# Kernel optimization log

Hardware: AMD Instinct MI355X
Metric: run time of the kernel (lower is better)

Reference implementation:

```python
import jax, jax.numpy as jnp
import numpy as np

N, F, H, F_ = 8192, 256, 2, 64
NEG_MASK = -1e10
LEAKY_SLOPE = 0.2


def setup_inputs() -> dict:
    key = jax.random.key(0)
    k0, k1, k2, k3 = jax.random.split(key, 4)
    X = jax.random.normal(k0, (N, F), jnp.float32)
    A = (jax.random.uniform(k1, (N, N)) < 0.01).astype(jnp.float32)
    A = jnp.maximum(A, jnp.eye(N, dtype=jnp.float32))
    W = jax.random.normal(k2, (H, F, F_), jnp.float32) * (1.0 / np.sqrt(F))
    b = jnp.zeros((H, F_), jnp.float32)
    a = jax.random.normal(k3, (H, F_), jnp.float32) * 0.1
    return {"X": X, "A": A, "W": W, "b": b, "a": a}


def reference(X, A, W, b, a):
    # per-head projected features: [H, N, F_]
    feats = jnp.einsum('nf,hfo->hno', X, W)
    # score[h,i,j] = sum_o feats[h,i,o] * feats[h,j,o] * a[h,o]
    # (identical math to Dot(axes=-1)([X_0*X_1, a^T]) without the [N,N,F_] tensor)
    scores = jnp.einsum('hno,hmo->hnm', feats * a[:, None, :], feats)
    scores = jax.nn.leaky_relu(scores, negative_slope=LEAKY_SLOPE)
    scores = scores + NEG_MASK * (1.0 - A)  # adjacency mask (broadcast over heads)
    attn = jax.nn.softmax(scores, axis=-1)  # [H, N, N]
    # dropout_rate=0 -> identity at inference
    out = jnp.einsum('hnm,hmo->hno', attn, feats) + b[:, None, :]  # [H, N, F_]
    out = jnp.transpose(out, (1, 0, 2)).reshape(X.shape[0], H * F_)  # concat heads
    return jax.nn.relu(out)
```

## Files before the change

kernel.cpp:

```cpp
#include <hip/hip_runtime.h>

#define NN 8192
#define FIN 256
#define FO 64
#define CAP 192

typedef float nf4 __attribute__((ext_vector_type(4)));

__global__ __launch_bounds__(256) void feats_kernel(
    const float* __restrict__ X,
    const float* __restrict__ W,
    float* __restrict__ feats)
{
    __shared__ float Ws[128*FO];
    __shared__ float Xs[32*132];
    const int h = blockIdx.y;
    const int row0 = blockIdx.x * 32;
    const int t = threadIdx.x;
    const int rg = t >> 4;
    const int c0 = (t & 15) << 2;
    float acc0[4] = {0.f,0.f,0.f,0.f};
    float acc1[4] = {0.f,0.f,0.f,0.f};

    for (int kp = 0; kp < 2; ++kp){
        const int kb = kp * 128;
        const float* Wh = W + h*FIN*FO + kb*FO;
        #pragma unroll
        for (int it=0; it<8; ++it){
            int flat = (it*256 + t)*4;
            *(float4*)&Ws[flat] = *(const float4*)&Wh[flat];
        }
        #pragma unroll
        for (int it=0; it<4; ++it){
            int flat = (it*256 + t)*4;
            int r = flat >> 7, f0 = flat & 127;
            *(float4*)&Xs[r*132 + f0] = *(const float4*)&X[(size_t)(row0+r)*FIN + kb + f0];
        }
        __syncthreads();
        const float* xp0 = &Xs[(rg*2+0)*132];
        const float* xp1 = &Xs[(rg*2+1)*132];
        #pragma unroll 4
        for (int k=0; k<128; ++k){
            float x0 = xp0[k], x1 = xp1[k];
            float4 w4 = *(const float4*)&Ws[k*FO + c0];
            acc0[0]=fmaf(x0,w4.x,acc0[0]); acc0[1]=fmaf(x0,w4.y,acc0[1]);
            acc0[2]=fmaf(x0,w4.z,acc0[2]); acc0[3]=fmaf(x0,w4.w,acc0[3]);
            acc1[0]=fmaf(x1,w4.x,acc1[0]); acc1[1]=fmaf(x1,w4.y,acc1[1]);
            acc1[2]=fmaf(x1,w4.z,acc1[2]); acc1[3]=fmaf(x1,w4.w,acc1[3]);
        }
        __syncthreads();
    }
    float* o0 = feats + ((size_t)(row0 + rg*2 + 0)*2 + h)*FO + c0;
    float* o1 = feats + ((size_t)(row0 + rg*2 + 1)*2 + h)*FO + c0;
    *(float4*)o0 = make_float4(acc0[0],acc0[1],acc0[2],acc0[3]);
    *(float4*)o1 = make_float4(acc1[0],acc1[1],acc1[2],acc1[3]);
}

__global__ __launch_bounds__(512) void gat_kernel(
    const float* __restrict__ A,
    const float* __restrict__ feats,
    const float* __restrict__ av,
    const float* __restrict__ bv,
    float* __restrict__ out)
{
    __shared__ int   nsh[CAP];
    __shared__ float s0[CAP], s1[CAP];
    __shared__ float part[8*128];
    __shared__ float red[2];
    __shared__ int   s_c;

    const int i = blockIdx.x, t = threadIdx.x;
    const int l  = t & 63;
    const int wv = t >> 6;
    const int gi = t >> 5, l32 = t & 31;

    float4 qa = *(const float4*)&av[l32*4];
    float4 qf = *(const float4*)&feats[(size_t)i*128 + l32*4];
    const float4 q4 = make_float4(qf.x*qa.x, qf.y*qa.y, qf.z*qa.z, qf.w*qa.w);

    if (t == 0) s_c = 0;
    __syncthreads();

    const nf4* Arow4 = (const nf4*)(A + (size_t)i*NN);
    nf4 v[4];
    #pragma unroll
    for (int r=0; r<4; ++r) v[r] = __builtin_nontemporal_load(&Arow4[r*512 + t]);

    const unsigned long long ltmask = (1ull << l) - 1ull;
    #pragma unroll
    for (int r=0; r<4; ++r){
        unsigned long long m0 = __ballot(v[r].x != 0.0f);
        unsigned long long m1 = __ballot(v[r].y != 0.0f);
        unsigned long long m2 = __ballot(v[r].z != 0.0f);
        unsigned long long m3 = __ballot(v[r].w != 0.0f);
        int p0 = __popcll(m0), p1 = __popcll(m1), p2 = __popcll(m2), p3 = __popcll(m3);
        int base = 0;
        if (l == 0) base = atomicAdd(&s_c, p0+p1+p2+p3);
        base = __shfl(base, 0, 64);
        const int colb = (r*512 + t)*4;
        if ((m0>>l)&1){ int p = base + __popcll(m0 & ltmask); if (p<CAP) nsh[p] = colb;   } base += p0;
        if ((m1>>l)&1){ int p = base + __popcll(m1 & ltmask); if (p<CAP) nsh[p] = colb+1; } base += p1;
        if ((m2>>l)&1){ int p = base + __popcll(m2 & ltmask); if (p<CAP) nsh[p] = colb+2; } base += p2;
        if ((m3>>l)&1){ int p = base + __popcll(m3 & ltmask); if (p<CAP) nsh[p] = colb+3; }
    }
    __syncthreads();
    const int n = min(s_c, CAP);

    for (int k0 = gi*4; k0 < n; k0 += 64){
        const int kn = min(4, n - k0);
        float4 f[4];
        #pragma unroll
        for (int u=0; u<4; ++u){
            int j = (u < kn) ? nsh[k0+u] : i;
            f[u] = *(const float4*)&feats[(size_t)j*128 + l32*4];
        }
        #pragma unroll
        for (int u=0; u<4; ++u){
            float d = f[u].x*q4.x + f[u].y*q4.y + f[u].z*q4.z + f[u].w*q4.w;
            d += __shfl_xor(d, 1, 64);
            d += __shfl_xor(d, 2, 64);
            d += __shfl_xor(d, 4, 64);
            d += __shfl_xor(d, 8, 64);
            d = (d >= 0.f) ? d : 0.2f*d;
            if (u < kn){
                if (l32 == 0)  s0[k0+u] = d;
                if (l32 == 16) s1[k0+u] = d;
            }
        }
    }
    __syncthreads();

    if (wv < 2){
        float* ss = wv ? s1 : s0;
        float m = -1e30f;
        for (int k=l; k<n; k+=64) m = fmaxf(m, ss[k]);
        #pragma unroll
        for (int off=32; off; off>>=1) m = fmaxf(m, __shfl_xor(m, off, 64));
        float sum = 0.f;
        for (int k=l; k<n; k+=64){ float p = __expf(ss[k]-m); ss[k] = p; sum += p; }
        #pragma unroll
        for (int off=32; off; off>>=1) sum += __shfl_xor(sum, off, 64);
        if (l == 0) red[wv] = sum;
    }
    __syncthreads();

    const int g8 = t >> 6;
    const int o2 = (t & 63) * 2;
    const float* ps = (o2 >= 64) ? s1 : s0;
    float2 acc = make_float2(0.f, 0.f);
    int k = g8;
    for (; k + 24 < n; k += 32){
        int j0 = nsh[k], j1 = nsh[k+8], j2 = nsh[k+16], j3 = nsh[k+24];
        float2 f0 = *(const float2*)&feats[(size_t)j0*128 + o2];
        float2 f1 = *(const float2*)&feats[(size_t)j1*128 + o2];
        float2 f2 = *(const float2*)&feats[(size_t)j2*128 + o2];
        float2 f3 = *(const float2*)&feats[(size_t)j3*128 + o2];
        float p0 = ps[k], p1 = ps[k+8], p2 = ps[k+16], p3 = ps[k+24];
        acc.x = fmaf(p0, f0.x, acc.x); acc.y = fmaf(p0, f0.y, acc.y);
        acc.x = fmaf(p1, f1.x, acc.x); acc.y = fmaf(p1, f1.y, acc.y);
        acc.x = fmaf(p2, f2.x, acc.x); acc.y = fmaf(p2, f2.y, acc.y);
        acc.x = fmaf(p3, f3.x, acc.x); acc.y = fmaf(p3, f3.y, acc.y);
    }
    for (; k < n; k += 8){
        int j = nsh[k];
        float2 f = *(const float2*)&feats[(size_t)j*128 + o2];
        float p = ps[k];
        acc.x = fmaf(p, f.x, acc.x); acc.y = fmaf(p, f.y, acc.y);
    }
    *(float2*)&part[g8*128 + o2] = acc;
    __syncthreads();

    if (t < 128){
        float num = part[t]       + part[128+t] + part[256+t] + part[384+t]
                  + part[512+t]   + part[640+t] + part[768+t] + part[896+t];
        float val = num / red[t>>6] + bv[t];
        out[(size_t)i*128 + t] = fmaxf(val, 0.f);
    }
}

extern "C" void kernel_launch(void* const* d_in, const int* in_sizes, int n_in,
                              void* d_out, int out_size, void* d_ws, size_t ws_size,
                              hipStream_t stream) {
    const float* X = (const float*)d_in[0];
    const float* A = (const float*)d_in[1];
    const float* W = (const float*)d_in[2];
    const float* b = (const float*)d_in[3];
    const float* a = (const float*)d_in[4];
    float* out = (float*)d_out;

    float* feats = (float*)d_ws;

    feats_kernel<<<dim3(NN/32, 2), 256, 0, stream>>>(X, W, feats);
    gat_kernel  <<<dim3(NN),       512, 0, stream>>>(A, feats, a, b, out);
}
```

Measured before the change: 392.7 us.

## Process one adjacency row per wavefront instead of per 512-thread block

Reassigns the GAT kernel so each 64-lane wavefront owns one row, with four rows per 256-thread block. The neighbour list is built with wave-local ballot prefix counts instead of a shared atomic counter, and every __syncthreads and the cross-wave partial reduction are removed. Softmax and aggregation run inside the wave, and the normalisation and bias are fused into the final store. The aim is to cut block-level synchronisation and reduction overhead in a kernel dominated by streaming the dense A matrix. The trade-off is less parallelism per row, since each wave now issues the whole 32 KB row read in sequential rounds and does all the neighbour gathers itself.

```diff
diff --git a/kernel.cpp b/kernel.cpp
--- a/kernel.cpp
+++ b/kernel.cpp
@@ -56,62 +56,61 @@
     *(float4*)o1 = make_float4(acc1[0],acc1[1],acc1[2],acc1[3]);
 }
 
-__global__ __launch_bounds__(512) void gat_kernel(
+__global__ __launch_bounds__(256) void gat_kernel(
     const float* __restrict__ A,
     const float* __restrict__ feats,
     const float* __restrict__ av,
     const float* __restrict__ bv,
     float* __restrict__ out)
 {
-    __shared__ int   nsh[CAP];
-    __shared__ float s0[CAP], s1[CAP];
-    __shared__ float part[8*128];
-    __shared__ float red[2];
-    __shared__ int   s_c;
+    __shared__ int   nsh[4][CAP];
+    __shared__ float sc[4][2][CAP];
 
-    const int i = blockIdx.x, t = threadIdx.x;
-    const int l  = t & 63;
-    const int wv = t >> 6;
-    const int gi = t >> 5, l32 = t & 31;
+    const int w   = threadIdx.x >> 6;
+    const int l   = threadIdx.x & 63;
+    const int i   = (blockIdx.x << 2) + w;
+    const int gi  = l >> 5;
+    const int l32 = l & 31;
+
+    int*   ns = nsh[w];
+    float* s0 = sc[w][0];
+    float* s1 = sc[w][1];
 
     float4 qa = *(const float4*)&av[l32*4];
     float4 qf = *(const float4*)&feats[(size_t)i*128 + l32*4];
     const float4 q4 = make_float4(qf.x*qa.x, qf.y*qa.y, qf.z*qa.z, qf.w*qa.w);
 
-    if (t == 0) s_c = 0;
-    __syncthreads();
+    const nf4* Arow4 = (const nf4*)(A + (size_t)i*NN);
+    const unsigned long long ltmask = (1ull << l) - 1ull;
+    int base = 0;
+    #pragma unroll 1
+    for (int round = 0; round < 4; ++round){
+        nf4 v[8];
+        #pragma unroll
+        for (int r=0; r<8; ++r)
+            v[r] = __builtin_nontemporal_load(&Arow4[(round*8+r)*64 + l]);
+        #pragma unroll
+        for (int r=0; r<8; ++r){
+            unsigned long long m0 = __ballot(v[r].x != 0.0f);
+            unsigned long long m1 = __ballot(v[r].y != 0.0f);
+            unsigned long long m2 = __ballot(v[r].z != 0.0f);
+            unsigned long long m3 = __ballot(v[r].w != 0.0f);
+            int p0 = __popcll(m0), p1 = __popcll(m1), p2 = __popcll(m2), p3 = __popcll(m3);
+            const int colb = ((round*8+r)*64 + l)*4;
+            if ((m0>>l)&1){ int p = base + __popcll(m0 & ltmask); if (p<CAP) ns[p] = colb;   } base += p0;
+            if ((m1>>l)&1){ int p = base + __popcll(m1 & ltmask); if (p<CAP) ns[p] = colb+1; } base += p1;
+            if ((m2>>l)&1){ int p = base + __popcll(m2 & ltmask); if (p<CAP) ns[p] = colb+2; } base += p2;
+            if ((m3>>l)&1){ int p = base + __popcll(m3 & ltmask); if (p<CAP) ns[p] = colb+3; } base += p3;
+        }
+    }
+    const int n = min(base, CAP);
 
-    const nf4* Arow4 = (const nf4*)(A + (size_t)i*NN);
-    nf4 v[4];
-    #pragma unroll
-    for (int r=0; r<4; ++r) v[r] = __builtin_nontemporal_load(&Arow4[r*512 + t]);
-
-    const unsigned long long ltmask = (1ull << l) - 1ull;
-    #pragma unroll
-    for (int r=0; r<4; ++r){
-        unsigned long long m0 = __ballot(v[r].x != 0.0f);
-        unsigned long long m1 = __ballot(v[r].y != 0.0f);
-        unsigned long long m2 = __ballot(v[r].z != 0.0f);
-        unsigned long long m3 = __ballot(v[r].w != 0.0f);
-        int p0 = __popcll(m0), p1 = __popcll(m1), p2 = __popcll(m2), p3 = __popcll(m3);
-        int base = 0;
-        if (l == 0) base = atomicAdd(&s_c, p0+p1+p2+p3);
-        base = __shfl(base, 0, 64);
-        const int colb = (r*512 + t)*4;
-        if ((m0>>l)&1){ int p = base + __popcll(m0 & ltmask); if (p<CAP) nsh[p] = colb;   } base += p0;
-        if ((m1>>l)&1){ int p = base + __popcll(m1 & ltmask); if (p<CAP) nsh[p] = colb+1; } base += p1;
-        if ((m2>>l)&1){ int p = base + __popcll(m2 & ltmask); if (p<CAP) nsh[p] = colb+2; } base += p2;
-        if ((m3>>l)&1){ int p = base + __popcll(m3 & ltmask); if (p<CAP) nsh[p] = colb+3; }
-    }
-    __syncthreads();
-    const int n = min(s_c, CAP);
-
-    for (int k0 = gi*4; k0 < n; k0 += 64){
+    for (int k0 = gi*4; k0 < n; k0 += 8){
         const int kn = min(4, n - k0);
         float4 f[4];
         #pragma unroll
         for (int u=0; u<4; ++u){
-            int j = (u < kn) ? nsh[k0+u] : i;
+            int j = (u < kn) ? ns[k0+u] : i;
             f[u] = *(const float4*)&feats[(size_t)j*128 + l32*4];
         }
         #pragma unroll
@@ -128,54 +127,46 @@
             }
         }
     }
-    __syncthreads();
 
-    if (wv < 2){
-        float* ss = wv ? s1 : s0;
-        float m = -1e30f;
-        for (int k=l; k<n; k+=64) m = fmaxf(m, ss[k]);
-        #pragma unroll
-        for (int off=32; off; off>>=1) m = fmaxf(m, __shfl_xor(m, off, 64));
-        float sum = 0.f;
-        for (int k=l; k<n; k+=64){ float p = __expf(ss[k]-m); ss[k] = p; sum += p; }
-        #pragma unroll
-        for (int off=32; off; off>>=1) sum += __shfl_xor(sum, off, 64);
-        if (l == 0) red[wv] = sum;
-    }
-    __syncthreads();
+    float* ss = (l < 32) ? s0 : s1;
+    float mx = -1e30f;
+    for (int k = l32; k < n; k += 32) mx = fmaxf(mx, ss[k]);
+    #pragma unroll
+    for (int off = 16; off; off >>= 1) mx = fmaxf(mx, __shfl_xor(mx, off, 64));
+    float sum = 0.f;
+    for (int k = l32; k < n; k += 32){ float p = __expf(ss[k] - mx); ss[k] = p; sum += p; }
+    #pragma unroll
+    for (int off = 16; off; off >>= 1) sum += __shfl_xor(sum, off, 64);
 
-    const int g8 = t >> 6;
-    const int o2 = (t & 63) * 2;
-    const float* ps = (o2 >= 64) ? s1 : s0;
+    const int o2 = l * 2;
+    const float* ps = ss;
     float2 acc = make_float2(0.f, 0.f);
-    int k = g8;
-    for (; k + 24 < n; k += 32){
-        int j0 = nsh[k], j1 = nsh[k+8], j2 = nsh[k+16], j3 = nsh[k+24];
+    int k = 0;
+    for (; k + 4 <= n; k += 4){
+        int j0 = ns[k], j1 = ns[k+1], j2 = ns[k+2], j3 = ns[k+3];
         float2 f0 = *(const float2*)&feats[(size_t)j0*128 + o2];
         float2 f1 = *(const float2*)&feats[(size_t)j1*128 + o2];
         float2 f2 = *(const float2*)&feats[(size_t)j2*128 + o2];
         float2 f3 = *(const float2*)&feats[(size_t)j3*128 + o2];
-        float p0 = ps[k], p1 = ps[k+8], p2 = ps[k+16], p3 = ps[k+24];
+        float p0 = ps[k], p1 = ps[k+1], p2 = ps[k+2], p3 = ps[k+3];
         acc.x = fmaf(p0, f0.x, acc.x); acc.y = fmaf(p0, f0.y, acc.y);
         acc.x = fmaf(p1, f1.x, acc.x); acc.y = fmaf(p1, f1.y, acc.y);
         acc.x = fmaf(p2, f2.x, acc.x); acc.y = fmaf(p2, f2.y, acc.y);
         acc.x = fmaf(p3, f3.x, acc.x); acc.y = fmaf(p3, f3.y, acc.y);
     }
-    for (; k < n; k += 8){
-        int j = nsh[k];
+    for (; k < n; ++k){
+        int j = ns[k];
         float2 f = *(const float2*)&feats[(size_t)j*128 + o2];
         float p = ps[k];
         acc.x = fmaf(p, f.x, acc.x); acc.y = fmaf(p, f.y, acc.y);
     }
-    *(float2*)&part[g8*128 + o2] = acc;
-    __syncthreads();
 
-    if (t < 128){
-        float num = part[t]       + part[128+t] + part[256+t] + part[384+t]
-                  + part[512+t]   + part[640+t] + part[768+t] + part[896+t];
-        float val = num / red[t>>6] + bv[t];
-        out[(size_t)i*128 + t] = fmaxf(val, 0.f);
-    }
+    float2 bb = *(const float2*)&bv[o2];
+    float inv = 1.0f / sum;
+    float2 r;
+    r.x = fmaxf(fmaf(acc.x, inv, bb.x), 0.f);
+    r.y = fmaxf(fmaf(acc.y, inv, bb.y), 0.f);
+    *(float2*)&out[(size_t)i*128 + o2] = r;
 }
 
 extern "C" void kernel_launch(void* const* d_in, const int* in_sizes, int n_in,
@@ -191,5 +182,5 @@
     float* feats = (float*)d_ws;
 
     feats_kernel<<<dim3(NN/32, 2), 256, 0, stream>>>(X, W, feats);
-    gat_kernel  <<<dim3(NN),       512, 0, stream>>>(A, feats, a, b, out);
+    gat_kernel  <<<dim3(NN/4),     256, 0, stream>>>(A, feats, a, b, out);
 }
```

Measured after the change: 392.2 us. Within noise of the previous version (-0.1%).
